# Optimization experiments

Hardware: AMD Instinct MI355X
Metric: run time of the kernel (lower is better)

## Reference

```python
import jax, jax.numpy as jnp
import numpy as np

BETA = 1.0

def setup_inputs() -> dict:
    key = jax.random.key(0)
    k1, k2 = jax.random.split(key)
    z = jax.random.normal(k1, (8, 8192, 64), dtype=jnp.float32)
    # codebook initialized as randn * sc (sc=0.001) in the original module
    codebook = jax.random.normal(k2, (1024, 64), dtype=jnp.float32) * 0.001
    return {"z": z, "codebook": codebook}

def reference(z, codebook):
    # squared euclidean distances: ||z||^2 + ||c||^2 - 2 z.c  -> [B, T, code_num]
    d = (jnp.sum(z ** 2, axis=-1, keepdims=True)
         + jnp.sum(codebook ** 2, axis=1)
         - 2.0 * jnp.einsum('btd,kd->btk', z, codebook))
    min_encoding_indices = jnp.argmin(d, axis=-1)            # [B, T] int
    # one-hot @ codebook is exactly a gather of nearest code vectors
    z_q = codebook[min_encoding_indices]                     # [B, T, D]
    sg = jax.lax.stop_gradient
    loss = jnp.mean((sg(z_q) - z) ** 2) + BETA * jnp.mean((z_q - sg(z)) ** 2)
    # straight-through estimator
    z_q_st = z + sg(z_q - z)
    return (z_q_st, min_encoding_indices, loss)
```

## Files before the change

kernel.cpp:

```cpp
#include <hip/hip_runtime.h>

#define TOKENS 65536
#define DIM 64
#define NCODE 1024
#define MARGIN 1e-5f
#define MARGINS (MARGIN * 2097152.0f)
#define FLAG_CAP 8192
#define TPG 16

#define OUT_IDX_OFF ((size_t)TOKENS * DIM)
#define OUT_LOSS_OFF (OUT_IDX_OFF + TOKENS)

#define WS_LOSS   0
#define WS_FLAGC  8
#define WS_DONEA  12
#define WS_DGRP   16
#define WS_BNORM  2064
#define WS_BNS    6160
#define WS_CHI    10256
#define WS_CLO    141328
#define WS_PACKED 272400
#define WS_FLAGS  337936

typedef __attribute__((ext_vector_type(8))) short short8;
typedef __attribute__((ext_vector_type(8))) _Float16 half8;
typedef __attribute__((ext_vector_type(4))) float f32x4;

static __device__ __forceinline__ half8 as_h8(short8 v) {
    return __builtin_bit_cast(half8, v);
}

__device__ __forceinline__ float np_sumsq64(const float* __restrict__ x) {
#pragma clang fp contract(off)
    float r[8];
#pragma unroll
    for (int j = 0; j < 8; ++j) r[j] = x[j] * x[j];
#pragma unroll
    for (int i = 8; i < 64; i += 8) {
#pragma unroll
        for (int j = 0; j < 8; ++j) {
            float sq = x[i + j] * x[i + j];
            r[j] = r[j] + sq;
        }
    }
    return ((r[0] + r[1]) + (r[2] + r[3])) + ((r[4] + r[5]) + (r[6] + r[7]));
}

__global__ __launch_bounds__(256) void vq_prep(
    const float* __restrict__ cb, unsigned short* __restrict__ chi,
    unsigned short* __restrict__ clo, float* __restrict__ bnorm,
    float* __restrict__ bns,
    unsigned int* __restrict__ ctrl ) {
    int tid = blockIdx.x * 256 + threadIdx.x;
    if (tid < 516) ctrl[tid] = 0u;
    int j = tid & 7;
    int L = (tid >> 3) & 63;
    int cs = tid >> 9;
    int s = cs & 1, c = cs >> 1;
    int code = c * 16 + (L & 15);
    int d = s * 32 + (L >> 4) * 8 + j;
    float v = -8192.0f * cb[(size_t)code * DIM + d];
    _Float16 h = (_Float16)v;
    float hf = (float)h;
    float lo;
    {
#pragma clang fp contract(off)
        lo = v - hf;
    }
    _Float16 l = (_Float16)lo;
    chi[tid] = __builtin_bit_cast(unsigned short, h);
    clo[tid] = __builtin_bit_cast(unsigned short, l);

    if (tid < NCODE) {
        float bn = np_sumsq64(cb + (size_t)tid * DIM);
        bnorm[tid] = bn;
        bns[tid] = bn * 2097152.0f;
    }
}

__device__ __forceinline__ void top2_merge(float& a1, float& a2, int& ai,
                                           float b1, float b2, int bi) {
    float n1 = fminf(a1, b1);
    float n2 = fminf(fmaxf(a1, b1), fminf(a2, b2));
    ai = (b1 < a1) ? bi : ai;
    a1 = n1; a2 = n2;
}

__global__ __launch_bounds__(256, 4) void vq_fast(
    const float* __restrict__ z, const float* __restrict__ cb,
    const unsigned short* __restrict__ cfrag_hi,
    const unsigned short* __restrict__ cfrag_lo,
    const float* __restrict__ bnorm_s, float* __restrict__ out,
    unsigned int* __restrict__ flag_count, int* __restrict__ flag_list,
    unsigned long long* __restrict__ packed_min,
    double* __restrict__ loss_sum, unsigned int flag_cap) {
    __shared__ short8 sh_hi[2][512];
    __shared__ short8 sh_lo[2][512];
    __shared__ float bn_lds[NCODE];
    __shared__ int s_best[64];
    __shared__ int s_flag[64];

    const int tid = threadIdx.x;
    const int lane = tid & 63;
    const int w = tid >> 6;
    const int t0 = blockIdx.x * 64;
    const int tw = t0 + w * 16;
    const int col = lane & 15;
    const int quad = lane >> 4;

    ((float4*)bn_lds)[tid] = ((const float4*)bnorm_s)[tid];

    half8 zhi[2], zlo[2];
#pragma unroll
    for (int s = 0; s < 2; ++s) {
        const float* zp = z + (size_t)(tw + col) * DIM + s * 32 + quad * 8;
        float4 f0 = ((const float4*)zp)[0];
        float4 f1 = ((const float4*)zp)[1];
        float f[8] = {f0.x, f0.y, f0.z, f0.w, f1.x, f1.y, f1.z, f1.w};
        half8 h, l;
#pragma unroll
        for (int j = 0; j < 8; ++j) {
            float sv = f[j] * 512.0f;
            _Float16 hh = (_Float16)sv;
            float hf = (float)hh;
            float lo;
            {
#pragma clang fp contract(off)
                lo = sv - hf;
            }
            h[j] = hh;
            l[j] = (_Float16)lo;
        }
        zhi[s] = h; zlo[s] = l;
    }

    const short8* CH = (const short8*)cfrag_hi;
    const short8* CL = (const short8*)cfrag_lo;

    {
        short8 a0 = CH[tid], a1 = CH[tid + 256];
        short8 b0 = CL[tid], b1 = CL[tid + 256];
        sh_hi[0][tid] = a0; sh_hi[0][tid + 256] = a1;
        sh_lo[0][tid] = b0; sh_lo[0][tid + 256] = b1;
    }
    __syncthreads();

    float m1 = 3.0e38f, m2 = 3.0e38f;
    int bi = 0;
    const int koff = quad * 4;

    for (int g = 0; g < 16; ++g) {
        const int buf = g & 1;
        short8 a0, a1, b0, b1;
        if (g < 15) {
            const int base = (g + 1) * 512 + tid;
            a0 = CH[base]; a1 = CH[base + 256];
            b0 = CL[base]; b1 = CL[base + 256];
        }
#pragma unroll
        for (int cc = 0; cc < 4; ++cc) {
            const int c = g * 4 + cc;
            short8 ch0 = sh_hi[buf][(cc * 2 + 0) * 64 + lane];
            short8 ch1 = sh_hi[buf][(cc * 2 + 1) * 64 + lane];
            short8 cl0 = sh_lo[buf][(cc * 2 + 0) * 64 + lane];
            short8 cl1 = sh_lo[buf][(cc * 2 + 1) * 64 + lane];
            const int cbase = c * 16 + koff;
            const f32x4 bn = *(const f32x4*)&bn_lds[cbase];
            f32x4 acc = bn;
            acc = __builtin_amdgcn_mfma_f32_16x16x32_f16(as_h8(ch0), zhi[0], acc, 0, 0, 0);
            acc = __builtin_amdgcn_mfma_f32_16x16x32_f16(as_h8(cl0), zhi[0], acc, 0, 0, 0);
            acc = __builtin_amdgcn_mfma_f32_16x16x32_f16(as_h8(ch0), zlo[0], acc, 0, 0, 0);
            acc = __builtin_amdgcn_mfma_f32_16x16x32_f16(as_h8(ch1), zhi[1], acc, 0, 0, 0);
            acc = __builtin_amdgcn_mfma_f32_16x16x32_f16(as_h8(cl1), zhi[1], acc, 0, 0, 0);
            acc = __builtin_amdgcn_mfma_f32_16x16x32_f16(as_h8(ch1), zlo[1], acc, 0, 0, 0);
#pragma unroll
            for (int i = 0; i < 4; ++i) {
                float u = acc[i];
                float om1 = m1;
                bool lt = u < om1;
                float fm = fminf(m2, u);
                m2 = lt ? om1 : fm;
                m1 = lt ? u : om1;
                bi = lt ? (cbase + i) : bi;
            }
        }
        if (g < 15) {
            sh_hi[buf ^ 1][tid] = a0; sh_hi[buf ^ 1][tid + 256] = a1;
            sh_lo[buf ^ 1][tid] = b0; sh_lo[buf ^ 1][tid + 256] = b1;
            __syncthreads();
        }
    }

    {
        float a1 = m1, a2 = m2;
        int ai = bi;
        {
            float o1 = __shfl_xor(a1, 16); float o2 = __shfl_xor(a2, 16);
            int oi = __shfl_xor(ai, 16);
            top2_merge(a1, a2, ai, o1, o2, oi);
        }
        {
            float o1 = __shfl_xor(a1, 32); float o2 = __shfl_xor(a2, 32);
            int oi = __shfl_xor(ai, 32);
            top2_merge(a1, a2, ai, o1, o2, oi);
        }
        if (quad == 0) {
            const int slot = w * 16 + col;
            int fl = (a2 - a1) < MARGINS;
            if (fl) {
                unsigned int pos = atomicAdd(flag_count, 1u);
                if (pos >= flag_cap) fl = 0;
                else {
                    flag_list[pos] = t0 + slot;
                    packed_min[pos] = ~0ull;
                }
            }
            s_best[slot] = ai;
            s_flag[slot] = fl;
        }
    }
    __syncthreads();

    const int et = tid >> 1, h = tid & 1;
    float loss_t = 0.0f;
    if (et < 64 && !s_flag[et]) {
        const int B = s_best[et];
        const float4* cq  = (const float4*)(cb + (size_t)B * DIM + h * 32);
        const float4* zq4 = (const float4*)(z + (size_t)(t0 + et) * DIM + h * 32);
        float4* o4 = (float4*)(out + (size_t)(t0 + et) * DIM + h * 32);
#pragma unroll
        for (int jj = 0; jj < 8; ++jj) {
#pragma clang fp contract(off)
            float4 cc = cq[jj];
            float4 zz = zq4[jj];
            float d0 = cc.x - zz.x, d1 = cc.y - zz.y;
            float d2 = cc.z - zz.z, d3 = cc.w - zz.w;
            float4 o;
            o.x = zz.x + d0; o.y = zz.y + d1;
            o.z = zz.z + d2; o.w = zz.w + d3;
            o4[jj] = o;
            loss_t = __fmaf_rn(d0, d0, loss_t);
            loss_t = __fmaf_rn(d1, d1, loss_t);
            loss_t = __fmaf_rn(d2, d2, loss_t);
            loss_t = __fmaf_rn(d3, d3, loss_t);
        }
        if (h == 0) out[OUT_IDX_OFF + t0 + et] = (float)B;
    }
#pragma unroll
    for (int off = 32; off > 0; off >>= 1)
        loss_t += __shfl_down(loss_t, off);
    if (lane == 0 && w < 2) atomicAdd(loss_sum, (double)loss_t);
}

__device__ __forceinline__ unsigned long long shfl_down_u64(unsigned long long v, int off) {
    unsigned int lo = (unsigned int)v, hi = (unsigned int)(v >> 32);
    lo = __shfl_down(lo, off);
    hi = __shfl_down(hi, off);
    return ((unsigned long long)hi << 32) | lo;
}

__global__ __launch_bounds__(256) void vq_exact_min(
    const float* __restrict__ z, const float* __restrict__ cb,
    const float* __restrict__ bnorm,
    const unsigned int* __restrict__ flag_count,
    const int* __restrict__ flag_list,
    unsigned long long* __restrict__ packed_min,
    unsigned int* __restrict__ done_grp, unsigned int* __restrict__ done_all,
    float* __restrict__ out, double* __restrict__ loss_sum,
    unsigned int flag_cap) {
    __shared__ float zsh[TPG * 68];
    __shared__ float szs[TPG];
    __shared__ unsigned int s_old;

    const int tid = threadIdx.x;
    const int w = tid >> 6;
    const int lane = tid & 63;
    unsigned int count = *flag_count;
    if (count > flag_cap) count = flag_cap;
    const unsigned int ngroups = (count + TPG - 1) / TPG;

    if (count == 0) {
        if (blockIdx.x == 0 && tid == 0) {
            double L = atomicAdd(loss_sum, 0.0);
            out[OUT_LOSS_OFF] = (float)(2.0 * L / (double)((size_t)TOKENS * DIM));
        }
        return;
    }

    const int q = blockIdx.x & 3;
    const unsigned int g = blockIdx.x >> 2;
    if (g >= ngroups) return;

    const int k = q * 256 + w * 64 + lane;

    float row[DIM];
    {
        const float4* c4 = (const float4*)(cb + (size_t)k * DIM);
#pragma unroll
        for (int j = 0; j < 16; ++j) {
            float4 v = c4[j];
            row[4 * j + 0] = v.x; row[4 * j + 1] = v.y;
            row[4 * j + 2] = v.z; row[4 * j + 3] = v.w;
        }
    }
    const float bnk = bnorm[k];

    {
        const int i = tid >> 2, part = tid & 3;
        if (i < TPG) {
            const unsigned int li = g * TPG + i;
            if (li < count) {
                const int t = flag_list[li];
                const float4* zp = (const float4*)(z + (size_t)t * DIM + part * 16);
                float4* dst = (float4*)(zsh + i * 68 + part * 16);
#pragma unroll
                for (int e = 0; e < 4; ++e) dst[e] = zp[e];
            }
        }
    }
    __syncthreads();
    if (tid < TPG) szs[tid] = np_sumsq64(zsh + tid * 68);
    __syncthreads();

    for (int tt = 0; tt < TPG; ++tt) {
        const unsigned int li = g * TPG + tt;
        const float* zp = zsh + tt * 68;
        float l16[16];
#pragma unroll
        for (int g2 = 0; g2 < 4; ++g2) {
            float4 v0 = ((const float4*)(zp + 4 * g2))[0];
            float4 v1 = ((const float4*)(zp + 16 + 4 * g2))[0];
            float4 v2 = ((const float4*)(zp + 32 + 4 * g2))[0];
            float4 v3 = ((const float4*)(zp + 48 + 4 * g2))[0];
            float a0[4] = {v0.x, v0.y, v0.z, v0.w};
            float a1[4] = {v1.x, v1.y, v1.z, v1.w};
            float a2[4] = {v2.x, v2.y, v2.z, v2.w};
            float a3[4] = {v3.x, v3.y, v3.z, v3.w};
#pragma unroll
            for (int e = 0; e < 4; ++e) {
#pragma clang fp contract(off)
                int jj = 4 * g2 + e;
                float acc = a3[e] * row[48 + jj];
                acc = __fmaf_rn(a2[e], row[32 + jj], acc);
                acc = __fmaf_rn(a1[e], row[16 + jj], acc);
                acc = __fmaf_rn(a0[e], row[jj],      acc);
                l16[jj] = acc;
            }
        }
        float e_np;
        {
#pragma clang fp contract(off)
#pragma unroll
            for (int jj = 0; jj < 8; ++jj) l16[jj] = l16[jj] + l16[jj + 8];
#pragma unroll
            for (int jj = 0; jj < 4; ++jj) l16[jj] = l16[jj] + l16[jj + 4];
            l16[0] = l16[0] + l16[2];
            l16[1] = l16[1] + l16[3];
            e_np = l16[0] + l16[1];
        }
        float dd;
        {
#pragma clang fp contract(off)
            float t1 = szs[tt] + bnk;
            float mm = 2.0f * e_np;
            dd = t1 - mm;
        }
        unsigned long long pk =
            ((unsigned long long)__float_as_uint(dd) << 10) | (unsigned int)k;
#pragma unroll
        for (int off = 32; off > 0; off >>= 1) {
            unsigned long long o = shfl_down_u64(pk, off);
            pk = (o < pk) ? o : pk;
        }
        if (lane == 0 && li < count)
            atomicMin(&packed_min[li], pk);
    }

    __threadfence();
    __syncthreads();
    if (tid == 0) s_old = atomicAdd(&done_grp[g], 1u);
    __syncthreads();
    if (s_old != 3u) return;
    __threadfence();

    for (int tt = w * (TPG / 4); tt < (w + 1) * (TPG / 4); ++tt) {
        const unsigned int li = g * TPG + tt;
        if (li >= count) break;
        const int t = flag_list[li];
        const unsigned long long pk = atomicAdd(&packed_min[li], 0ull);
        const int best = (int)(pk & 1023ull);
        const float zl = zsh[tt * 68 + lane];
        const float zq = cb[(size_t)best * DIM + lane];
        float d, o;
        {
#pragma clang fp contract(off)
            d = zq - zl;
            o = zl + d;
        }
        out[(size_t)t * DIM + lane] = o;
        float l2 = d * d;
#pragma unroll
        for (int off = 32; off > 0; off >>= 1)
            l2 += __shfl_down(l2, off);
        if (lane == 0) {
            out[OUT_IDX_OFF + t] = (float)best;
            atomicAdd(loss_sum, (double)l2);
        }
    }

    __threadfence();
    __syncthreads();
    if (tid == 0) {
        unsigned int old = atomicAdd(done_all, 1u);
        if (old == ngroups - 1) {
            double L = atomicAdd(loss_sum, 0.0);
            out[OUT_LOSS_OFF] = (float)(2.0 * L / (double)((size_t)TOKENS * DIM));
        }
    }
}

extern "C" void kernel_launch(void* const* d_in, const int* in_sizes, int n_in,
                              void* d_out, int out_size, void* d_ws, size_t ws_size,
                              hipStream_t stream) {
    const float* z  = (const float*)d_in[0];
    const float* cb = (const float*)d_in[1];
    float* out = (float*)d_out;

    char* ws = (char*)d_ws;
    double* loss_sum = (double*)(ws + WS_LOSS);
    unsigned int* flag_count = (unsigned int*)(ws + WS_FLAGC);
    unsigned int* done_all = (unsigned int*)(ws + WS_DONEA);
    unsigned int* done_grp = (unsigned int*)(ws + WS_DGRP);
    float* bnorm = (float*)(ws + WS_BNORM);
    float* bns = (float*)(ws + WS_BNS);
    unsigned short* chi = (unsigned short*)(ws + WS_CHI);
    unsigned short* clo = (unsigned short*)(ws + WS_CLO);
    unsigned long long* packed = (unsigned long long*)(ws + WS_PACKED);
    int* flag_list = (int*)(ws + WS_FLAGS);

    unsigned int cap = 0;
    if (ws_size > WS_FLAGS + 4) {
        size_t c = (ws_size - WS_FLAGS) / 4;
        cap = (c > FLAG_CAP) ? FLAG_CAP : (unsigned int)c;
    }

    vq_prep<<<dim3(256), dim3(256), 0, stream>>>(
        cb, chi, clo, bnorm, bns, (unsigned int*)ws);
    vq_fast<<<dim3(TOKENS / 64), dim3(256), 0, stream>>>(
        z, cb, chi, clo, bns, out, flag_count, flag_list, packed, loss_sum, cap);
    vq_exact_min<<<dim3(2048), dim3(256), 0, stream>>>(
        z, cb, bnorm, flag_count, flag_list, packed, done_grp, done_all,
        out, loss_sum, cap);
}
```

Baseline: 142.7 us.

## Split codebook across wave pairs, halve tokens per block, merge partial top-2 in LDS

Each block now handles 32 tokens instead of 64. Pairs of waves share a 16-token tile and each scans half of the codebook, then the partial top-2 results are merged through shared memory. Shared-memory staging shrinks and the norms are read straight from global memory, and launch bounds request 8 blocks per CU. The aim is more waves in flight and a shorter serial loop per wave. The cost is that every codebook fragment is reloaded from global/L2 by twice as many blocks, plus an extra barrier and merge step.

```diff
diff --git a/kernel.cpp b/kernel.cpp
--- a/kernel.cpp
+++ b/kernel.cpp
@@ -86,7 +86,7 @@
     a1 = n1; a2 = n2;
 }
 
-__global__ __launch_bounds__(256, 4) void vq_fast(
+__global__ __launch_bounds__(256, 8) void vq_fast(
     const float* __restrict__ z, const float* __restrict__ cb,
     const unsigned short* __restrict__ cfrag_hi,
     const unsigned short* __restrict__ cfrag_lo,
@@ -94,21 +94,22 @@
     unsigned int* __restrict__ flag_count, int* __restrict__ flag_list,
     unsigned long long* __restrict__ packed_min,
     double* __restrict__ loss_sum, unsigned int flag_cap) {
-    __shared__ short8 sh_hi[2][512];
-    __shared__ short8 sh_lo[2][512];
-    __shared__ float bn_lds[NCODE];
-    __shared__ int s_best[64];
-    __shared__ int s_flag[64];
+    __shared__ short8 sh_hi[2][256];
+    __shared__ short8 sh_lo[2][256];
+    __shared__ float s_m1[64], s_m2[64];
+    __shared__ int s_bi[64];
+    __shared__ int s_best[32];
+    __shared__ int s_flag[32];
 
     const int tid = threadIdx.x;
     const int lane = tid & 63;
     const int w = tid >> 6;
-    const int t0 = blockIdx.x * 64;
-    const int tw = t0 + w * 16;
+    const int h = w & 1;
+    const int tt = w >> 1;
+    const int t0 = blockIdx.x * 32;
+    const int tw = t0 + tt * 16;
     const int col = lane & 15;
     const int quad = lane >> 4;
-
-    ((float4*)bn_lds)[tid] = ((const float4*)bnorm_s)[tid];
 
     half8 zhi[2], zlo[2];
 #pragma unroll
@@ -117,7 +118,7 @@
         float4 f0 = ((const float4*)zp)[0];
         float4 f1 = ((const float4*)zp)[1];
         float f[8] = {f0.x, f0.y, f0.z, f0.w, f1.x, f1.y, f1.z, f1.w};
-        half8 h, l;
+        half8 hh8, ll8;
 #pragma unroll
         for (int j = 0; j < 8; ++j) {
             float sv = f[j] * 512.0f;
@@ -128,20 +129,23 @@
 #pragma clang fp contract(off)
                 lo = sv - hf;
             }
-            h[j] = hh;
-            l[j] = (_Float16)lo;
-        }
-        zhi[s] = h; zlo[s] = l;
+            hh8[j] = hh;
+            ll8[j] = (_Float16)lo;
+        }
+        zhi[s] = hh8; zlo[s] = ll8;
     }
 
     const short8* CH = (const short8*)cfrag_hi;
     const short8* CL = (const short8*)cfrag_lo;
+    const f32x4* bnp = (const f32x4*)bnorm_s;
+
+    const int sc = tid >> 7;
+    const int st = tid & 127;
 
     {
-        short8 a0 = CH[tid], a1 = CH[tid + 256];
-        short8 b0 = CL[tid], b1 = CL[tid + 256];
-        sh_hi[0][tid] = a0; sh_hi[0][tid + 256] = a1;
-        sh_lo[0][tid] = b0; sh_lo[0][tid + 256] = b1;
+        const int c0 = sc * 32;
+        sh_hi[0][tid] = CH[c0 * 128 + st];
+        sh_lo[0][tid] = CL[c0 * 128 + st];
     }
     __syncthreads();
 
@@ -149,44 +153,44 @@
     int bi = 0;
     const int koff = quad * 4;
 
-    for (int g = 0; g < 16; ++g) {
+    f32x4 nbn = bnp[(h * 32) * 4 + quad];
+
+    for (int g = 0; g < 32; ++g) {
         const int buf = g & 1;
-        short8 a0, a1, b0, b1;
-        if (g < 15) {
-            const int base = (g + 1) * 512 + tid;
-            a0 = CH[base]; a1 = CH[base + 256];
-            b0 = CL[base]; b1 = CL[base + 256];
-        }
-#pragma unroll
-        for (int cc = 0; cc < 4; ++cc) {
-            const int c = g * 4 + cc;
-            short8 ch0 = sh_hi[buf][(cc * 2 + 0) * 64 + lane];
-            short8 ch1 = sh_hi[buf][(cc * 2 + 1) * 64 + lane];
-            short8 cl0 = sh_lo[buf][(cc * 2 + 0) * 64 + lane];
-            short8 cl1 = sh_lo[buf][(cc * 2 + 1) * 64 + lane];
-            const int cbase = c * 16 + koff;
-            const f32x4 bn = *(const f32x4*)&bn_lds[cbase];
-            f32x4 acc = bn;
-            acc = __builtin_amdgcn_mfma_f32_16x16x32_f16(as_h8(ch0), zhi[0], acc, 0, 0, 0);
-            acc = __builtin_amdgcn_mfma_f32_16x16x32_f16(as_h8(cl0), zhi[0], acc, 0, 0, 0);
-            acc = __builtin_amdgcn_mfma_f32_16x16x32_f16(as_h8(ch0), zlo[0], acc, 0, 0, 0);
-            acc = __builtin_amdgcn_mfma_f32_16x16x32_f16(as_h8(ch1), zhi[1], acc, 0, 0, 0);
-            acc = __builtin_amdgcn_mfma_f32_16x16x32_f16(as_h8(cl1), zhi[1], acc, 0, 0, 0);
-            acc = __builtin_amdgcn_mfma_f32_16x16x32_f16(as_h8(ch1), zlo[1], acc, 0, 0, 0);
-#pragma unroll
-            for (int i = 0; i < 4; ++i) {
-                float u = acc[i];
-                float om1 = m1;
-                bool lt = u < om1;
-                float fm = fminf(m2, u);
-                m2 = lt ? om1 : fm;
-                m1 = lt ? u : om1;
-                bi = lt ? (cbase + i) : bi;
-            }
-        }
-        if (g < 15) {
-            sh_hi[buf ^ 1][tid] = a0; sh_hi[buf ^ 1][tid + 256] = a1;
-            sh_lo[buf ^ 1][tid] = b0; sh_lo[buf ^ 1][tid + 256] = b1;
+        short8 a0, b0;
+        if (g < 31) {
+            const int cn = sc * 32 + g + 1;
+            a0 = CH[cn * 128 + st];
+            b0 = CL[cn * 128 + st];
+        }
+        const int c = h * 32 + g;
+        short8 ch0 = sh_hi[buf][h * 128 + lane];
+        short8 ch1 = sh_hi[buf][h * 128 + 64 + lane];
+        short8 cl0 = sh_lo[buf][h * 128 + lane];
+        short8 cl1 = sh_lo[buf][h * 128 + 64 + lane];
+        const f32x4 bn = nbn;
+        if (g < 31) nbn = bnp[(c + 1) * 4 + quad];
+        const int cbase = c * 16 + koff;
+        f32x4 acc = bn;
+        acc = __builtin_amdgcn_mfma_f32_16x16x32_f16(as_h8(ch0), zhi[0], acc, 0, 0, 0);
+        acc = __builtin_amdgcn_mfma_f32_16x16x32_f16(as_h8(cl0), zhi[0], acc, 0, 0, 0);
+        acc = __builtin_amdgcn_mfma_f32_16x16x32_f16(as_h8(ch0), zlo[0], acc, 0, 0, 0);
+        acc = __builtin_amdgcn_mfma_f32_16x16x32_f16(as_h8(ch1), zhi[1], acc, 0, 0, 0);
+        acc = __builtin_amdgcn_mfma_f32_16x16x32_f16(as_h8(cl1), zhi[1], acc, 0, 0, 0);
+        acc = __builtin_amdgcn_mfma_f32_16x16x32_f16(as_h8(ch1), zlo[1], acc, 0, 0, 0);
+#pragma unroll
+        for (int i = 0; i < 4; ++i) {
+            float u = acc[i];
+            float om1 = m1;
+            bool lt = u < om1;
+            float fm = fminf(m2, u);
+            m2 = lt ? om1 : fm;
+            m1 = lt ? u : om1;
+            bi = lt ? (cbase + i) : bi;
+        }
+        if (g < 31) {
+            sh_hi[buf ^ 1][tid] = a0;
+            sh_lo[buf ^ 1][tid] = b0;
             __syncthreads();
         }
     }
@@ -205,29 +209,40 @@
             top2_merge(a1, a2, ai, o1, o2, oi);
         }
         if (quad == 0) {
-            const int slot = w * 16 + col;
-            int fl = (a2 - a1) < MARGINS;
-            if (fl) {
-                unsigned int pos = atomicAdd(flag_count, 1u);
-                if (pos >= flag_cap) fl = 0;
-                else {
-                    flag_list[pos] = t0 + slot;
-                    packed_min[pos] = ~0ull;
-                }
+            const int idx = tt * 32 + h * 16 + col;
+            s_m1[idx] = a1; s_m2[idx] = a2; s_bi[idx] = ai;
+        }
+    }
+    __syncthreads();
+
+    if (tid < 32) {
+        const int jt = tid >> 4, jc = tid & 15;
+        const int i0 = jt * 32 + jc;
+        const int i1 = jt * 32 + 16 + jc;
+        float a1 = s_m1[i0], a2 = s_m2[i0];
+        int ai = s_bi[i0];
+        top2_merge(a1, a2, ai, s_m1[i1], s_m2[i1], s_bi[i1]);
+        int fl = (a2 - a1) < MARGINS;
+        if (fl) {
+            unsigned int pos = atomicAdd(flag_count, 1u);
+            if (pos >= flag_cap) fl = 0;
+            else {
+                flag_list[pos] = t0 + tid;
+                packed_min[pos] = ~0ull;
             }
-            s_best[slot] = ai;
-            s_flag[slot] = fl;
-        }
-    }
-    __syncthreads();
-
-    const int et = tid >> 1, h = tid & 1;
+        }
+        s_best[tid] = ai;
+        s_flag[tid] = fl;
+    }
+    __syncthreads();
+
+    const int et = tid >> 1, eh = tid & 1;
     float loss_t = 0.0f;
-    if (et < 64 && !s_flag[et]) {
+    if (et < 32 && !s_flag[et]) {
         const int B = s_best[et];
-        const float4* cq  = (const float4*)(cb + (size_t)B * DIM + h * 32);
-        const float4* zq4 = (const float4*)(z + (size_t)(t0 + et) * DIM + h * 32);
-        float4* o4 = (float4*)(out + (size_t)(t0 + et) * DIM + h * 32);
+        const float4* cq  = (const float4*)(cb + (size_t)B * DIM + eh * 32);
+        const float4* zq4 = (const float4*)(z + (size_t)(t0 + et) * DIM + eh * 32);
+        float4* o4 = (float4*)(out + (size_t)(t0 + et) * DIM + eh * 32);
 #pragma unroll
         for (int jj = 0; jj < 8; ++jj) {
 #pragma clang fp contract(off)
@@ -244,12 +259,12 @@
             loss_t = __fmaf_rn(d2, d2, loss_t);
             loss_t = __fmaf_rn(d3, d3, loss_t);
         }
-        if (h == 0) out[OUT_IDX_OFF + t0 + et] = (float)B;
+        if (eh == 0) out[OUT_IDX_OFF + t0 + et] = (float)B;
     }
 #pragma unroll
     for (int off = 32; off > 0; off >>= 1)
         loss_t += __shfl_down(loss_t, off);
-    if (lane == 0 && w < 2) atomicAdd(loss_sum, (double)loss_t);
+    if (lane == 0 && w == 0) atomicAdd(loss_sum, (double)loss_t);
 }
 
 __device__ __forceinline__ unsigned long long shfl_down_u64(unsigned long long v, int off) {
@@ -446,7 +461,7 @@
 
     vq_prep<<<dim3(256), dim3(256), 0, stream>>>(
         cb, chi, clo, bnorm, bns, (unsigned int*)ws);
-    vq_fast<<<dim3(TOKENS / 64), dim3(256), 0, stream>>>(
+    vq_fast<<<dim3(TOKENS / 32), dim3(256), 0, stream>>>(
         z, cb, chi, clo, bns, out, flag_count, flag_list, packed, loss_sum, cap);
     vq_exact_min<<<dim3(2048), dim3(256), 0, stream>>>(
         z, cb, bnorm, flag_count, flag_list, packed, done_grp, done_all,
```

New measurement: 142.3 us. Within noise of the previous version (-0.3%).
